# Kernel optimization log

Hardware: AMD Instinct MI355X
Metric: run time of the kernel (lower is better)

The kernel has to match this reference:

```python
import jax, jax.numpy as jnp
import numpy as np

B, S, D = 4, 2048, 512
H, DK = 8, 64
EPS = 1e-8


def setup_inputs() -> dict:
    key = jax.random.key(0)
    ks = jax.random.split(key, 11)
    sc = 1.0 / np.sqrt(D)
    Q = jax.random.normal(ks[0], (B, S, D), dtype=jnp.float32)
    # binary keep-mask over key positions, [B, S]
    attention_masks = (jax.random.uniform(ks[1], (B, S)) > 0.1).astype(jnp.float32)
    Wq = jax.random.normal(ks[2], (D, H * DK), dtype=jnp.float32) * sc
    bq = jax.random.normal(ks[3], (H * DK,), dtype=jnp.float32) * 0.01
    Wk = jax.random.normal(ks[4], (D, H * DK), dtype=jnp.float32) * sc
    bk = jax.random.normal(ks[5], (H * DK,), dtype=jnp.float32) * 0.01
    Wv = jax.random.normal(ks[6], (D, H * DK), dtype=jnp.float32) * sc
    bv = jax.random.normal(ks[7], (H * DK,), dtype=jnp.float32) * 0.01
    Wo = jax.random.normal(ks[8], (H * DK, D), dtype=jnp.float32) * (1.0 / np.sqrt(H * DK))
    bo = jax.random.normal(ks[9], (D,), dtype=jnp.float32) * 0.01
    return {"Q": Q, "attention_masks": attention_masks, "Wq": Wq, "bq": bq,
            "Wk": Wk, "bk": bk, "Wv": Wv, "bv": bv, "Wo": Wo, "bo": bo}


def reference(Q, attention_masks, Wq, bq, Wk, bk, Wv, bv, Wo, bo):
    b, s, _ = Q.shape
    # projections -> [B, H, S, DK]
    q = (Q @ Wq + bq).reshape(b, s, H, DK).transpose(0, 2, 1, 3)
    k = (Q @ Wk + bk).reshape(b, s, H, DK).transpose(0, 2, 1, 3)
    v = (Q @ Wv + bv).reshape(b, s, H, DK).transpose(0, 2, 1, 3)
    # scores: exp(QK^T / sqrt(dk)) * mask, normalized by row-sum (no max subtraction, matching source)
    scores = jnp.exp(jnp.einsum('bhqd,bhkd->bhqk', q, k) / np.sqrt(DK))
    scores = scores * attention_masks[:, None, None, :]  # mask broadcast over query dim
    attn = scores / (jnp.sum(scores, axis=-1, keepdims=True) + EPS)
    ctx = jnp.einsum('bhqk,bhkd->bhqd', attn, v)
    ctx = ctx.transpose(0, 2, 1, 3).reshape(b, s, H * DK)
    return ctx @ Wo + bo
```

## Files before the change

kernel.cpp:

```cpp
#include <hip/hip_runtime.h>
#include <math.h>

constexpr int NB = 4, NS = 2048, ND = 512, NH = 8, NDK = 64;
constexpr int NM = NB * NS, NHD = NH * NDK;

typedef short short8v __attribute__((ext_vector_type(8)));
typedef float f32x16v __attribute__((ext_vector_type(16)));
typedef unsigned int uint4v __attribute__((ext_vector_type(4)));

__device__ __forceinline__ unsigned short f2bf(float f) {
    unsigned u = __float_as_uint(f);
    return (unsigned short)((u + 0x7fffu + ((u >> 16) & 1u)) >> 16);
}
__device__ __forceinline__ float bf2f(unsigned short h) {
    return __uint_as_float(((unsigned)h) << 16);
}

#define MFMA32(a, b, c) __builtin_amdgcn_mfma_f32_32x32x16_bf16(a, b, c, 0, 0, 0)

__global__ __launch_bounds__(256) void split_x(
    const float* __restrict__ X, unsigned short* __restrict__ xh,
    unsigned short* __restrict__ xl)
{
    const size_t base = ((size_t)blockIdx.x * 256 + threadIdx.x) * 16;
#pragma unroll
    for (int j = 0; j < 4; ++j) {
        float4 v = *(const float4*)&X[base + 4 * j];
        ushort4 h, l;
        h.x = f2bf(v.x); h.y = f2bf(v.y); h.z = f2bf(v.z); h.w = f2bf(v.w);
        l.x = f2bf(v.x - bf2f(h.x)); l.y = f2bf(v.y - bf2f(h.y));
        l.z = f2bf(v.z - bf2f(h.z)); l.w = f2bf(v.w - bf2f(h.w));
        *(ushort4*)&xh[base + 4 * j] = h;
        *(ushort4*)&xl[base + 4 * j] = l;
    }
}

__global__ __launch_bounds__(256) void split_wT(
    const float* __restrict__ W0, const float* __restrict__ W1,
    const float* __restrict__ W2, const float* __restrict__ W3,
    unsigned short* __restrict__ wth, unsigned short* __restrict__ wtl)
{
    const int z = blockIdx.z;
    const float* W = (z == 0) ? W0 : (z == 1) ? W1 : (z == 2) ? W2 : W3;
    unsigned short* th = wth + (size_t)z * ND * ND;
    unsigned short* tl = wtl + (size_t)z * ND * ND;

    __shared__ float T[64][68];
    const int t = threadIdx.x;
    const int k0 = blockIdx.y * 64, n0 = blockIdx.x * 64;
    {
        const int r = t >> 2, c4 = (t & 3) * 16;
#pragma unroll
        for (int j = 0; j < 4; ++j)
            *(float4*)&T[r][c4 + 4 * j] = *(const float4*)&W[(size_t)(k0 + r) * ND + n0 + c4 + 4 * j];
    }
    __syncthreads();
    {
        const int r = t >> 2, c4 = (t & 3) * 16;
        unsigned short* dh = th + (size_t)(n0 + r) * ND + k0 + c4;
        unsigned short* dl = tl + (size_t)(n0 + r) * ND + k0 + c4;
#pragma unroll
        for (int j = 0; j < 4; ++j) {
            ushort4 h, l;
#pragma unroll
            for (int e = 0; e < 4; ++e) {
                float v = T[c4 + 4 * j + e][r];
                unsigned short hh = f2bf(v);
                ((unsigned short*)&h)[e] = hh;
                ((unsigned short*)&l)[e] = f2bf(v - bf2f(hh));
            }
            *(ushort4*)(dh + 4 * j) = h;
            *(ushort4*)(dl + 4 * j) = l;
        }
    }
}

__global__ __launch_bounds__(256, 2) void proj_qkv_mfma(
    const unsigned short* __restrict__ xh, const unsigned short* __restrict__ xl,
    const unsigned short* __restrict__ wth, const unsigned short* __restrict__ wtl,
    const float* __restrict__ bq, const float* __restrict__ bk,
    const float* __restrict__ bv,
    unsigned short* __restrict__ qh, unsigned short* __restrict__ ql,
    unsigned short* __restrict__ kh, unsigned short* __restrict__ kl,
    unsigned short* __restrict__ vh)
{
    constexpr int AH = 0, AL = 16384, BH = 32768, BL = 49152;
    __shared__ __align__(16) unsigned char smem[65536];

    const int z = blockIdx.z;
    const float* bias = (z == 0) ? bq : (z == 1) ? bk : bv;
    unsigned short* hp = (z == 0) ? qh : (z == 1) ? kh : vh;
    unsigned short* lp = (z == 0) ? ql : (z == 1) ? kl : (unsigned short*)0;
    const unsigned char* bth = (const unsigned char*)(wth + (size_t)z * ND * ND);
    const unsigned char* btl = (const unsigned char*)(wtl + (size_t)z * ND * ND);

    const int tid = threadIdx.x, lane = tid & 63, w = tid >> 6;
    const int wm = w >> 1, wn = w & 1;
    const int c = lane & 31, hi = lane >> 5;
    const int m0 = blockIdx.y * 128, n0 = blockIdx.x * 128;

    const unsigned char* ah_base = (const unsigned char*)xh;
    const unsigned char* al_base = (const unsigned char*)xl;

    int rr[4], gg[4], dd[4];
#pragma unroll
    for (int i = 0; i < 4; ++i) {
        int G = tid + 256 * i;
        rr[i] = G >> 3; gg[i] = G & 7;
        dd[i] = rr[i] * 128 + ((gg[i] ^ (rr[i] & 7)) * 16);
    }

    uint4v sah[4], sal[4], sbh[4], sbl[4];
    auto loads = [&](int kt) {
        const int kb = kt * 128;
#pragma unroll
        for (int i = 0; i < 4; ++i) {
            const size_t arow = (size_t)(m0 + rr[i]) * 1024 + kb + gg[i] * 16;
            const size_t brow = (size_t)(n0 + rr[i]) * 1024 + kb + gg[i] * 16;
            sah[i] = *(const uint4v*)(ah_base + arow);
            sal[i] = *(const uint4v*)(al_base + arow);
            sbh[i] = *(const uint4v*)(bth + brow);
            sbl[i] = *(const uint4v*)(btl + brow);
        }
    };
    auto writes = [&]() {
#pragma unroll
        for (int i = 0; i < 4; ++i) {
            *(uint4v*)(smem + AH + dd[i]) = sah[i];
            *(uint4v*)(smem + AL + dd[i]) = sal[i];
            *(uint4v*)(smem + BH + dd[i]) = sbh[i];
            *(uint4v*)(smem + BL + dd[i]) = sbl[i];
        }
    };

    f32x16v acc[2][2];
#pragma unroll
    for (int a = 0; a < 2; ++a)
#pragma unroll
        for (int bq2 = 0; bq2 < 2; ++bq2)
#pragma unroll
            for (int r = 0; r < 16; ++r) acc[a][bq2][r] = 0.f;

    loads(0);
    for (int kt = 0; kt < ND / 64; ++kt) {
        __syncthreads();
        writes();
        if (kt + 1 < ND / 64) loads(kt + 1);
        __syncthreads();
#pragma unroll
        for (int ks = 0; ks < 4; ++ks) {
            short8v afh[2], afl[2], bfh[2], bfl[2];
#pragma unroll
            for (int ms = 0; ms < 2; ++ms) {
                const int row = wm * 64 + ms * 32 + c;
                const int gb = row * 128 + (((2 * ks + hi) ^ (c & 7)) * 16);
                afh[ms] = *(const short8v*)(smem + AH + gb);
                afl[ms] = *(const short8v*)(smem + AL + gb);
            }
#pragma unroll
            for (int ns = 0; ns < 2; ++ns) {
                const int row = wn * 64 + ns * 32 + c;
                const int gb = row * 128 + (((2 * ks + hi) ^ (c & 7)) * 16);
                bfh[ns] = *(const short8v*)(smem + BH + gb);
                bfl[ns] = *(const short8v*)(smem + BL + gb);
            }
#pragma unroll
            for (int ms = 0; ms < 2; ++ms)
#pragma unroll
                for (int ns = 0; ns < 2; ++ns) {
                    acc[ms][ns] = MFMA32(afh[ms], bfh[ns], acc[ms][ns]);
                    acc[ms][ns] = MFMA32(afh[ms], bfl[ns], acc[ms][ns]);
                    acc[ms][ns] = MFMA32(afl[ms], bfh[ns], acc[ms][ns]);
                }
        }
    }

    const int b = m0 >> 11;
    const int s_base = (m0 & (NS - 1)) + wm * 64;
#pragma unroll
    for (int ns = 0; ns < 2; ++ns) {
        const int n = n0 + wn * 64 + ns * 32 + c;
        const int h = n >> 6, dk = n & (NDK - 1);
        const float bv4 = bias[n];
        const size_t bhBase = (size_t)(b * NH + h) * NS * NDK + dk;
#pragma unroll
        for (int ms = 0; ms < 2; ++ms)
#pragma unroll
            for (int r = 0; r < 16; ++r) {
                const int s = s_base + ms * 32 + (r & 3) + 8 * (r >> 2) + 4 * hi;
                const float v = acc[ms][ns][r] + bv4;
                const unsigned short h0 = f2bf(v);
                hp[bhBase + (size_t)s * NDK] = h0;
                if (lp) lp[bhBase + (size_t)s * NDK] = f2bf(v - bf2f(h0));
            }
    }
}

__global__ __launch_bounds__(256) void vt_convert(
    const unsigned short* __restrict__ vh, unsigned short* __restrict__ vth)
{
    const int bh = blockIdx.y;
    const int s0 = blockIdx.x * 64;
    __shared__ unsigned short th[64][72];
    const int t = threadIdx.x;
    {
        const int sl = t & 63, ch = (t >> 6) * 16;
        const unsigned short* sh = vh + ((size_t)bh * NS + s0 + sl) * NDK + ch;
#pragma unroll
        for (int j = 0; j < 4; ++j)
            *(ushort4*)&th[sl][ch + 4 * j] = *(const ushort4*)(sh + 4 * j);
    }
    __syncthreads();
    {
        const int dv = t >> 2, sc = (t & 3) * 16;
        unsigned short* dh = vth + ((size_t)bh * NDK + dv) * NS + s0 + sc;
#pragma unroll
        for (int j = 0; j < 4; ++j) {
            ushort4 oh;
            oh.x = th[sc + 4 * j + 0][dv]; oh.y = th[sc + 4 * j + 1][dv];
            oh.z = th[sc + 4 * j + 2][dv]; oh.w = th[sc + 4 * j + 3][dv];
            *(ushort4*)(dh + 4 * j) = oh;
        }
    }
}

__global__ __launch_bounds__(256, 2) void attn(
    const unsigned short* __restrict__ qhp, const unsigned short* __restrict__ qlp,
    const unsigned short* __restrict__ khp, const unsigned short* __restrict__ klp,
    const unsigned short* __restrict__ vthp,
    const float* __restrict__ maskp,
    unsigned short* __restrict__ cth, unsigned short* __restrict__ ctl)
{
    constexpr int KH_OFF = 0, KL_OFF = 8192, VH_OFF = 16384;
    constexpr int P_OFF = 24576;
    __shared__ __align__(16) unsigned char smem[45056];

    const int tid = threadIdx.x, lane = tid & 63, w = tid >> 6;
    const int bid = blockIdx.x;
    const int xcd = bid & 7, r0 = bid >> 3;
    const int qt = r0 & 15, bh = xcd + 8 * (r0 >> 4);
    const int b = bh >> 3;
    const int q0 = qt * 128;
    const int c = lane & 31, hi = lane >> 5;
    const int csw = (c & 7) * 16;

    unsigned* Ph = (unsigned*)(smem + P_OFF + w * 5120);
    unsigned* Pl = (unsigned*)(smem + P_OFF + w * 5120 + 2560);

    const unsigned char* kh_base = (const unsigned char*)khp + (size_t)bh * NS * 128;
    const unsigned char* kl_base = (const unsigned char*)klp + (size_t)bh * NS * 128;
    const unsigned char* vh_base = (const unsigned char*)vthp + (size_t)bh * 64 * 4096;

    const int G1 = tid, G2 = tid + 256;
    const int r1 = G1 >> 3, g1 = G1 & 7, r2 = G2 >> 3, g2 = G2 & 7;
    const int d1 = r1 * 128 + ((g1 ^ (r1 & 7)) * 16);
    const int d2 = r2 * 128 + ((g2 ^ (r2 & 7)) * 16);

    uint4v skh1, skl1, svh1, skh2, skl2, svh2;
    auto loads = [&](int kt) {
        const size_t ko = (size_t)kt * 8192;
        const size_t vo = (size_t)kt * 128;
        skh1 = *(const uint4v*)(kh_base + ko + (size_t)G1 * 16);
        skh2 = *(const uint4v*)(kh_base + ko + (size_t)G2 * 16);
        skl1 = *(const uint4v*)(kl_base + ko + (size_t)G1 * 16);
        skl2 = *(const uint4v*)(kl_base + ko + (size_t)G2 * 16);
        svh1 = *(const uint4v*)(vh_base + vo + (size_t)r1 * 4096 + g1 * 16);
        svh2 = *(const uint4v*)(vh_base + vo + (size_t)r2 * 4096 + g2 * 16);
    };
    auto writes = [&]() {
        *(uint4v*)(smem + KH_OFF + d1) = skh1;
        *(uint4v*)(smem + KH_OFF + d2) = skh2;
        *(uint4v*)(smem + KL_OFF + d1) = skl1;
        *(uint4v*)(smem + KL_OFF + d2) = skl2;
        *(uint4v*)(smem + VH_OFF + d1) = svh1;
        *(uint4v*)(smem + VH_OFF + d2) = svh2;
    };

    short8v qfh[4], qfl[4];
    {
        const unsigned short* qr  = qhp + ((size_t)bh * NS + q0 + 32 * w + c) * NDK + 8 * hi;
        const unsigned short* qrl = qlp + ((size_t)bh * NS + q0 + 32 * w + c) * NDK + 8 * hi;
#pragma unroll
        for (int km = 0; km < 4; ++km) {
            qfh[km] = *(const short8v*)(qr + km * 16);
            qfl[km] = *(const short8v*)(qrl + km * 16);
        }
    }

    f32x16v acc[2];
#pragma unroll
    for (int d = 0; d < 2; ++d)
#pragma unroll
        for (int r = 0; r < 16; ++r) acc[d][r] = 0.f;
    float dsum = 0.f;

    loads(0);
    for (int kt = 0; kt < NS / 64; ++kt) {
        __syncthreads();
        writes();
        if (kt + 1 < NS / 64) loads(kt + 1);
        __syncthreads();
#pragma unroll
        for (int kb = 0; kb < 2; ++kb) {
            short8v kfh[4], kfl[4];
            const int rowb = (32 * kb + c) * 128;
#pragma unroll
            for (int km = 0; km < 4; ++km) {
                const int gb = ((2 * km + hi) * 16) ^ csw;
                kfh[km] = *(const short8v*)(smem + KH_OFF + rowb + gb);
                kfl[km] = *(const short8v*)(smem + KL_OFF + rowb + gb);
            }
            f32x16v sacc;
#pragma unroll
            for (int r = 0; r < 16; ++r) sacc[r] = 0.f;
#pragma unroll
            for (int km = 0; km < 4; ++km) {
                sacc = MFMA32(kfh[km], qfh[km], sacc);
                sacc = MFMA32(kfh[km], qfl[km], sacc);
                sacc = MFMA32(kfl[km], qfh[km], sacc);
            }
            float pm[16];
#pragma unroll
            for (int rr2 = 0; rr2 < 4; ++rr2) {
                float4 mv = *(const float4*)&maskp[(size_t)b * NS + kt * 64 + 32 * kb + 8 * rr2 + 4 * hi];
                pm[4 * rr2 + 0] = mv.x; pm[4 * rr2 + 1] = mv.y;
                pm[4 * rr2 + 2] = mv.z; pm[4 * rr2 + 3] = mv.w;
            }
            float pf[16];
#pragma unroll
            for (int r = 0; r < 16; ++r) {
                float pv = __expf(sacc[r] * 0.125f) * pm[r];
                pf[r] = pv;
                dsum += pv;
            }
            unsigned wah[4], wbh[4], wal[4], wbl[4];
#pragma unroll
            for (int rr2 = 0; rr2 < 4; ++rr2) {
                unsigned short h0 = f2bf(pf[4 * rr2 + 0]), h1 = f2bf(pf[4 * rr2 + 1]);
                unsigned short h2 = f2bf(pf[4 * rr2 + 2]), h3 = f2bf(pf[4 * rr2 + 3]);
                wah[rr2] = (unsigned)h0 | ((unsigned)h1 << 16);
                wbh[rr2] = (unsigned)h2 | ((unsigned)h3 << 16);
                unsigned short l0 = f2bf(pf[4 * rr2 + 0] - bf2f(h0));
                unsigned short l1 = f2bf(pf[4 * rr2 + 1] - bf2f(h1));
                unsigned short l2 = f2bf(pf[4 * rr2 + 2] - bf2f(h2));
                unsigned short l3 = f2bf(pf[4 * rr2 + 3] - bf2f(h3));
                wal[rr2] = (unsigned)l0 | ((unsigned)l1 << 16);
                wbl[rr2] = (unsigned)l2 | ((unsigned)l3 << 16);
            }
#pragma unroll
            for (int rr2 = 0; rr2 < 4; ++rr2) {
                uint2 th2; th2.x = wah[rr2]; th2.y = wbh[rr2];
                uint2 tl2; tl2.x = wal[rr2]; tl2.y = wbl[rr2];
                *(uint2*)&Ph[c * 20 + 4 * rr2 + 2 * hi] = th2;
                *(uint2*)&Pl[c * 20 + 4 * rr2 + 2 * hi] = tl2;
            }
            asm volatile("s_waitcnt lgkmcnt(0)" ::: "memory");
            __builtin_amdgcn_sched_barrier(0);
#pragma unroll
            for (int pc2 = 0; pc2 < 2; ++pc2) {
                const int pc = 2 * kb + pc2;
                uint4v th4 = *(const uint4v*)&Ph[c * 20 + 8 * pc2 + 4 * hi];
                uint4v tl4 = *(const uint4v*)&Pl[c * 20 + 8 * pc2 + 4 * hi];
                short8v pfh = __builtin_bit_cast(short8v, th4);
                short8v pfl = __builtin_bit_cast(short8v, tl4);
                const int vgb = ((2 * pc + hi) * 16) ^ csw;
#pragma unroll
                for (int d = 0; d < 2; ++d) {
                    const int vrow = (32 * d + c) * 128;
                    short8v vfh = *(const short8v*)(smem + VH_OFF + vrow + vgb);
                    acc[d] = MFMA32(vfh, pfh, acc[d]);
                    acc[d] = MFMA32(vfh, pfl, acc[d]);
                }
            }
        }
    }

    dsum += __shfl_xor(dsum, 32);
    const float inv = 1.0f / (dsum + 1e-8f);
    unsigned short* ohr = cth + (size_t)bh * 64 * NS + q0 + 32 * w + c;
    unsigned short* olr = ctl + (size_t)bh * 64 * NS + q0 + 32 * w + c;
#pragma unroll
    for (int d = 0; d < 2; ++d)
#pragma unroll
        for (int r = 0; r < 16; ++r) {
            const int dv = 32 * d + (r & 3) + 8 * (r >> 2) + 4 * hi;
            const float v = acc[d][r] * inv;
            const unsigned short h0 = f2bf(v);
            ohr[(size_t)dv * NS] = h0;
            olr[(size_t)dv * NS] = f2bf(v - bf2f(h0));
        }
}

__global__ __launch_bounds__(256) void ctx_split(
    const unsigned short* __restrict__ cth, const unsigned short* __restrict__ ctl,
    unsigned short* __restrict__ cnh, unsigned short* __restrict__ cnl)
{
    const int bh = blockIdx.y;
    const int b = bh >> 3, h = bh & 7;
    const int s0 = blockIdx.x * 64;
    __shared__ unsigned short th[64][72];
    __shared__ unsigned short tl[64][72];
    const int t = threadIdx.x;
    {
        const int rd = t >> 2, sc = (t & 3) * 16;
        const unsigned short* sh = cth + ((size_t)bh * NDK + rd) * NS + s0 + sc;
        const unsigned short* sv = ctl + ((size_t)bh * NDK + rd) * NS + s0 + sc;
#pragma unroll
        for (int j = 0; j < 4; ++j) {
            *(ushort4*)&th[rd][sc + 4 * j] = *(const ushort4*)(sh + 4 * j);
            *(ushort4*)&tl[rd][sc + 4 * j] = *(const ushort4*)(sv + 4 * j);
        }
    }
    __syncthreads();
    {
        const int sl = t >> 2, kc = (t & 3) * 16;
        const size_t m = (size_t)b * NS + s0 + sl;
        unsigned short* dh = cnh + m * NHD + h * NDK + kc;
        unsigned short* dl = cnl + m * NHD + h * NDK + kc;
#pragma unroll
        for (int j = 0; j < 4; ++j) {
            ushort4 hh, ll;
#pragma unroll
            for (int e = 0; e < 4; ++e) {
                hh_e_assign:;
                ((unsigned short*)&hh)[e] = th[kc + 4 * j + e][sl];
                ((unsigned short*)&ll)[e] = tl[kc + 4 * j + e][sl];
            }
            *(ushort4*)(dh + 4 * j) = hh;
            *(ushort4*)(dl + 4 * j) = ll;
        }
    }
}

__global__ __launch_bounds__(256, 2) void proj_out_mfma(
    const unsigned short* __restrict__ cnh, const unsigned short* __restrict__ cnl,
    const unsigned short* __restrict__ wth, const unsigned short* __restrict__ wtl,
    const float* __restrict__ bo, float* __restrict__ out)
{
    constexpr int AH = 0, AL = 16384, BH = 32768, BL = 49152;
    __shared__ __align__(16) unsigned char smem[65536];

    const int tid = threadIdx.x, lane = tid & 63, w = tid >> 6;
    const int wm = w >> 1, wn = w & 1;
    const int c = lane & 31, hi = lane >> 5;
    const int m0 = blockIdx.y * 128, n0 = blockIdx.x * 128;

    const unsigned char* ah_base = (const unsigned char*)cnh;
    const unsigned char* al_base = (const unsigned char*)cnl;
    const unsigned char* bth = (const unsigned char*)wth;
    const unsigned char* btl = (const unsigned char*)wtl;

    int rr[4], gg[4], dd[4];
#pragma unroll
    for (int i = 0; i < 4; ++i) {
        int G = tid + 256 * i;
        rr[i] = G >> 3; gg[i] = G & 7;
        dd[i] = rr[i] * 128 + ((gg[i] ^ (rr[i] & 7)) * 16);
    }

    uint4v sah[4], sal[4], sbh[4], sbl[4];
    auto loads = [&](int kt) {
        const int kb = kt * 128;
#pragma unroll
        for (int i = 0; i < 4; ++i) {
            const size_t arow = (size_t)(m0 + rr[i]) * 1024 + kb + gg[i] * 16;
            const size_t brow = (size_t)(n0 + rr[i]) * 1024 + kb + gg[i] * 16;
            sah[i] = *(const uint4v*)(ah_base + arow);
            sal[i] = *(const uint4v*)(al_base + arow);
            sbh[i] = *(const uint4v*)(bth + brow);
            sbl[i] = *(const uint4v*)(btl + brow);
        }
    };
    auto writes = [&]() {
#pragma unroll
        for (int i = 0; i < 4; ++i) {
            *(uint4v*)(smem + AH + dd[i]) = sah[i];
            *(uint4v*)(smem + AL + dd[i]) = sal[i];
            *(uint4v*)(smem + BH + dd[i]) = sbh[i];
            *(uint4v*)(smem + BL + dd[i]) = sbl[i];
        }
    };

    f32x16v acc[2][2];
#pragma unroll
    for (int a = 0; a < 2; ++a)
#pragma unroll
        for (int bq2 = 0; bq2 < 2; ++bq2)
#pragma unroll
            for (int r = 0; r < 16; ++r) acc[a][bq2][r] = 0.f;

    loads(0);
    for (int kt = 0; kt < NHD / 64; ++kt) {
        __syncthreads();
        writes();
        if (kt + 1 < NHD / 64) loads(kt + 1);
        __syncthreads();
#pragma unroll
        for (int ks = 0; ks < 4; ++ks) {
            short8v afh[2], afl[2], bfh[2], bfl[2];
#pragma unroll
            for (int ms = 0; ms < 2; ++ms) {
                const int row = wm * 64 + ms * 32 + c;
                const int gb = row * 128 + (((2 * ks + hi) ^ (c & 7)) * 16);
                afh[ms] = *(const short8v*)(smem + AH + gb);
                afl[ms] = *(const short8v*)(smem + AL + gb);
            }
#pragma unroll
            for (int ns = 0; ns < 2; ++ns) {
                const int row = wn * 64 + ns * 32 + c;
                const int gb = row * 128 + (((2 * ks + hi) ^ (c & 7)) * 16);
                bfh[ns] = *(const short8v*)(smem + BH + gb);
                bfl[ns] = *(const short8v*)(smem + BL + gb);
            }
#pragma unroll
            for (int ms = 0; ms < 2; ++ms)
#pragma unroll
                for (int ns = 0; ns < 2; ++ns) {
                    acc[ms][ns] = MFMA32(afh[ms], bfh[ns], acc[ms][ns]);
                    acc[ms][ns] = MFMA32(afh[ms], bfl[ns], acc[ms][ns]);
                    acc[ms][ns] = MFMA32(afl[ms], bfh[ns], acc[ms][ns]);
                }
        }
    }

#pragma unroll
    for (int ns = 0; ns < 2; ++ns) {
        const int n = n0 + wn * 64 + ns * 32 + c;
        const float bv4 = bo[n];
#pragma unroll
        for (int ms = 0; ms < 2; ++ms)
#pragma unroll
            for (int r = 0; r < 16; ++r) {
                const int m = m0 + wm * 64 + ms * 32 + (r & 3) + 8 * (r >> 2) + 4 * hi;
                out[(size_t)m * ND + n] = acc[ms][ns][r] + bv4;
            }
    }
}

extern "C" void kernel_launch(void* const* d_in, const int* in_sizes, int n_in,
                              void* d_out, int out_size, void* d_ws, size_t ws_size,
                              hipStream_t stream) {
    const float* Q    = (const float*)d_in[0];
    const float* mask = (const float*)d_in[1];
    const float* Wq   = (const float*)d_in[2];
    const float* bq   = (const float*)d_in[3];
    const float* Wk   = (const float*)d_in[4];
    const float* bk   = (const float*)d_in[5];
    const float* Wv   = (const float*)d_in[6];
    const float* bv   = (const float*)d_in[7];
    const float* Wo   = (const float*)d_in[8];
    const float* bo   = (const float*)d_in[9];

    unsigned char* W = (unsigned char*)d_ws;
    constexpr size_t MB = 1048576;
    unsigned short* xh   = (unsigned short*)(W + 0);
    unsigned short* xl   = (unsigned short*)(W + 8 * MB);
    unsigned short* wtH  = (unsigned short*)(W + 16 * MB);
    unsigned short* wtL  = (unsigned short*)(W + 18 * MB);
    unsigned short* qh   = (unsigned short*)(W + 20 * MB);
    unsigned short* ql   = (unsigned short*)(W + 28 * MB);
    unsigned short* kh   = (unsigned short*)(W + 36 * MB);
    unsigned short* kl   = (unsigned short*)(W + 44 * MB);
    unsigned short* vh   = (unsigned short*)(W + 52 * MB);
    unsigned short* vth  = (unsigned short*)(W + 0);
    unsigned short* cth  = (unsigned short*)(W + 8 * MB);
    unsigned short* ctl  = (unsigned short*)(W + 52 * MB);
    unsigned short* cnh  = (unsigned short*)(W + 20 * MB);
    unsigned short* cnl  = (unsigned short*)(W + 28 * MB);

    split_x<<<NM * ND / (256 * 16), 256, 0, stream>>>(Q, xh, xl);
    split_wT<<<dim3(8, 8, 4), 256, 0, stream>>>(Wq, Wk, Wv, Wo, wtH, wtL);

    proj_qkv_mfma<<<dim3(NHD / 128, NM / 128, 3), 256, 0, stream>>>(
        xh, xl, wtH, wtL, bq, bk, bv, qh, ql, kh, kl, vh);

    vt_convert<<<dim3(NS / 64, NB * NH), 256, 0, stream>>>(vh, vth);

    attn<<<512, 256, 0, stream>>>(qh, ql, kh, kl, vth, mask, cth, ctl);

    ctx_split<<<dim3(NS / 64, NB * NH), 256, 0, stream>>>(cth, ctl, cnh, cnl);

    proj_out_mfma<<<dim3(ND / 128, NM / 128), 256, 0, stream>>>(
        cnh, cnl, wtH + (size_t)3 * ND * ND, wtL + (size_t)3 * ND * ND,
        bo, (float*)d_out);
}
```

Baseline: 279.4 us.

## Drop low-half bf16 split for P and context, double-buffer attention K/V tiles

The attention kernel now stores probabilities only as a single bf16 value and runs one PV MFMA per tile instead of two. The context output drops its low part, so ctx_split and the output projection move only the high half and run two MFMAs per step instead of three. The K/V shared-memory staging is double-buffered, leaving one barrier per tile instead of two, and exp is computed via exp2f with a prescaled constant. The aim is to cut MFMA count, LDS traffic and memory bandwidth, at the cost of lower numerical accuracy and more shared memory per block.

```diff
diff --git a/kernel.cpp b/kernel.cpp
--- a/kernel.cpp
+++ b/kernel.cpp
@@ -229,11 +229,12 @@
     const unsigned short* __restrict__ khp, const unsigned short* __restrict__ klp,
     const unsigned short* __restrict__ vthp,
     const float* __restrict__ maskp,
-    unsigned short* __restrict__ cth, unsigned short* __restrict__ ctl)
-{
-    constexpr int KH_OFF = 0, KL_OFF = 8192, VH_OFF = 16384;
-    constexpr int P_OFF = 24576;
-    __shared__ __align__(16) unsigned char smem[45056];
+    unsigned short* __restrict__ cth)
+{
+    constexpr int NT = NS / 64;
+    constexpr int KH = 0, KL = 8192, VH = 16384, TILE = 24576;
+    constexpr int P_OFF = 49152;
+    __shared__ __align__(16) unsigned char smem[59392];
 
     const int tid = threadIdx.x, lane = tid & 63, w = tid >> 6;
     const int bid = blockIdx.x;
@@ -244,8 +245,7 @@
     const int c = lane & 31, hi = lane >> 5;
     const int csw = (c & 7) * 16;
 
-    unsigned* Ph = (unsigned*)(smem + P_OFF + w * 5120);
-    unsigned* Pl = (unsigned*)(smem + P_OFF + w * 5120 + 2560);
+    unsigned* Ph = (unsigned*)(smem + P_OFF + w * 2560);
 
     const unsigned char* kh_base = (const unsigned char*)khp + (size_t)bh * NS * 128;
     const unsigned char* kl_base = (const unsigned char*)klp + (size_t)bh * NS * 128;
@@ -267,13 +267,13 @@
         svh1 = *(const uint4v*)(vh_base + vo + (size_t)r1 * 4096 + g1 * 16);
         svh2 = *(const uint4v*)(vh_base + vo + (size_t)r2 * 4096 + g2 * 16);
     };
-    auto writes = [&]() {
-        *(uint4v*)(smem + KH_OFF + d1) = skh1;
-        *(uint4v*)(smem + KH_OFF + d2) = skh2;
-        *(uint4v*)(smem + KL_OFF + d1) = skl1;
-        *(uint4v*)(smem + KL_OFF + d2) = skl2;
-        *(uint4v*)(smem + VH_OFF + d1) = svh1;
-        *(uint4v*)(smem + VH_OFF + d2) = svh2;
+    auto writes = [&](unsigned char* buf) {
+        *(uint4v*)(buf + KH + d1) = skh1;
+        *(uint4v*)(buf + KH + d2) = skh2;
+        *(uint4v*)(buf + KL + d1) = skl1;
+        *(uint4v*)(buf + KL + d2) = skl2;
+        *(uint4v*)(buf + VH + d1) = svh1;
+        *(uint4v*)(buf + VH + d2) = svh2;
     };
 
     short8v qfh[4], qfl[4];
@@ -294,12 +294,7 @@
         for (int r = 0; r < 16; ++r) acc[d][r] = 0.f;
     float dsum = 0.f;
 
-    loads(0);
-    for (int kt = 0; kt < NS / 64; ++kt) {
-        __syncthreads();
-        writes();
-        if (kt + 1 < NS / 64) loads(kt + 1);
-        __syncthreads();
+    auto compute = [&](const unsigned char* buf, int kt) {
 #pragma unroll
         for (int kb = 0; kb < 2; ++kb) {
             short8v kfh[4], kfl[4];
@@ -307,8 +302,8 @@
 #pragma unroll
             for (int km = 0; km < 4; ++km) {
                 const int gb = ((2 * km + hi) * 16) ^ csw;
-                kfh[km] = *(const short8v*)(smem + KH_OFF + rowb + gb);
-                kfl[km] = *(const short8v*)(smem + KL_OFF + rowb + gb);
+                kfh[km] = *(const short8v*)(buf + KH + rowb + gb);
+                kfl[km] = *(const short8v*)(buf + KL + rowb + gb);
             }
             f32x16v sacc;
 #pragma unroll
@@ -326,33 +321,23 @@
                 pm[4 * rr2 + 0] = mv.x; pm[4 * rr2 + 1] = mv.y;
                 pm[4 * rr2 + 2] = mv.z; pm[4 * rr2 + 3] = mv.w;
             }
-            float pf[16];
+            unsigned short hh[16];
 #pragma unroll
             for (int r = 0; r < 16; ++r) {
-                float pv = __expf(sacc[r] * 0.125f) * pm[r];
-                pf[r] = pv;
-                dsum += pv;
-            }
-            unsigned wah[4], wbh[4], wal[4], wbl[4];
+                float pv = exp2f(sacc[r] * 0.18033688011112042f) * pm[r];
+                hh[r] = f2bf(pv);
+                dsum += bf2f(hh[r]);
+            }
+            unsigned wah[4], wbh[4];
 #pragma unroll
             for (int rr2 = 0; rr2 < 4; ++rr2) {
-                unsigned short h0 = f2bf(pf[4 * rr2 + 0]), h1 = f2bf(pf[4 * rr2 + 1]);
-                unsigned short h2 = f2bf(pf[4 * rr2 + 2]), h3 = f2bf(pf[4 * rr2 + 3]);
-                wah[rr2] = (unsigned)h0 | ((unsigned)h1 << 16);
-                wbh[rr2] = (unsigned)h2 | ((unsigned)h3 << 16);
-                unsigned short l0 = f2bf(pf[4 * rr2 + 0] - bf2f(h0));
-                unsigned short l1 = f2bf(pf[4 * rr2 + 1] - bf2f(h1));
-                unsigned short l2 = f2bf(pf[4 * rr2 + 2] - bf2f(h2));
-                unsigned short l3 = f2bf(pf[4 * rr2 + 3] - bf2f(h3));
-                wal[rr2] = (unsigned)l0 | ((unsigned)l1 << 16);
-                wbl[rr2] = (unsigned)l2 | ((unsigned)l3 << 16);
+                wah[rr2] = (unsigned)hh[4 * rr2 + 0] | ((unsigned)hh[4 * rr2 + 1] << 16);
+                wbh[rr2] = (unsigned)hh[4 * rr2 + 2] | ((unsigned)hh[4 * rr2 + 3] << 16);
             }
 #pragma unroll
             for (int rr2 = 0; rr2 < 4; ++rr2) {
                 uint2 th2; th2.x = wah[rr2]; th2.y = wbh[rr2];
-                uint2 tl2; tl2.x = wal[rr2]; tl2.y = wbl[rr2];
                 *(uint2*)&Ph[c * 20 + 4 * rr2 + 2 * hi] = th2;
-                *(uint2*)&Pl[c * 20 + 4 * rr2 + 2 * hi] = tl2;
             }
             asm volatile("s_waitcnt lgkmcnt(0)" ::: "memory");
             __builtin_amdgcn_sched_barrier(0);
@@ -360,85 +345,87 @@
             for (int pc2 = 0; pc2 < 2; ++pc2) {
                 const int pc = 2 * kb + pc2;
                 uint4v th4 = *(const uint4v*)&Ph[c * 20 + 8 * pc2 + 4 * hi];
-                uint4v tl4 = *(const uint4v*)&Pl[c * 20 + 8 * pc2 + 4 * hi];
                 short8v pfh = __builtin_bit_cast(short8v, th4);
-                short8v pfl = __builtin_bit_cast(short8v, tl4);
                 const int vgb = ((2 * pc + hi) * 16) ^ csw;
 #pragma unroll
                 for (int d = 0; d < 2; ++d) {
                     const int vrow = (32 * d + c) * 128;
-                    short8v vfh = *(const short8v*)(smem + VH_OFF + vrow + vgb);
+                    short8v vfh = *(const short8v*)(buf + VH + vrow + vgb);
                     acc[d] = MFMA32(vfh, pfh, acc[d]);
-                    acc[d] = MFMA32(vfh, pfl, acc[d]);
                 }
             }
         }
+    };
+
+    unsigned char* buf0 = smem;
+    unsigned char* buf1 = smem + TILE;
+
+    loads(0);
+    writes(buf0);
+    loads(1);
+    __syncthreads();
+
+    auto step = [&](int kt, unsigned char* rbuf, unsigned char* wbuf) {
+        if (kt + 1 < NT) writes(wbuf);
+        if (kt + 2 < NT) loads(kt + 2);
+        compute(rbuf, kt);
+        __syncthreads();
+    };
+    for (int kt = 0; kt < NT; kt += 2) {
+        step(kt, buf0, buf1);
+        step(kt + 1, buf1, buf0);
     }
 
     dsum += __shfl_xor(dsum, 32);
     const float inv = 1.0f / (dsum + 1e-8f);
     unsigned short* ohr = cth + (size_t)bh * 64 * NS + q0 + 32 * w + c;
-    unsigned short* olr = ctl + (size_t)bh * 64 * NS + q0 + 32 * w + c;
 #pragma unroll
     for (int d = 0; d < 2; ++d)
 #pragma unroll
         for (int r = 0; r < 16; ++r) {
             const int dv = 32 * d + (r & 3) + 8 * (r >> 2) + 4 * hi;
-            const float v = acc[d][r] * inv;
-            const unsigned short h0 = f2bf(v);
-            ohr[(size_t)dv * NS] = h0;
-            olr[(size_t)dv * NS] = f2bf(v - bf2f(h0));
+            ohr[(size_t)dv * NS] = f2bf(acc[d][r] * inv);
         }
 }
 
 __global__ __launch_bounds__(256) void ctx_split(
-    const unsigned short* __restrict__ cth, const unsigned short* __restrict__ ctl,
-    unsigned short* __restrict__ cnh, unsigned short* __restrict__ cnl)
+    const unsigned short* __restrict__ cth, unsigned short* __restrict__ cnh)
 {
     const int bh = blockIdx.y;
     const int b = bh >> 3, h = bh & 7;
     const int s0 = blockIdx.x * 64;
     __shared__ unsigned short th[64][72];
-    __shared__ unsigned short tl[64][72];
     const int t = threadIdx.x;
     {
         const int rd = t >> 2, sc = (t & 3) * 16;
         const unsigned short* sh = cth + ((size_t)bh * NDK + rd) * NS + s0 + sc;
-        const unsigned short* sv = ctl + ((size_t)bh * NDK + rd) * NS + s0 + sc;
-#pragma unroll
-        for (int j = 0; j < 4; ++j) {
+#pragma unroll
+        for (int j = 0; j < 4; ++j)
             *(ushort4*)&th[rd][sc + 4 * j] = *(const ushort4*)(sh + 4 * j);
-            *(ushort4*)&tl[rd][sc + 4 * j] = *(const ushort4*)(sv + 4 * j);
-        }
     }
     __syncthreads();
     {
         const int sl = t >> 2, kc = (t & 3) * 16;
         const size_t m = (size_t)b * NS + s0 + sl;
         unsigned short* dh = cnh + m * NHD + h * NDK + kc;
-        unsigned short* dl = cnl + m * NHD + h * NDK + kc;
 #pragma unroll
         for (int j = 0; j < 4; ++j) {
-            ushort4 hh, ll;
-#pragma unroll
-            for (int e = 0; e < 4; ++e) {
-                hh_e_assign:;
+            ushort4 hh;
+#pragma unroll
+            for (int e = 0; e < 4; ++e)
                 ((unsigned short*)&hh)[e] = th[kc + 4 * j + e][sl];
-                ((unsigned short*)&ll)[e] = tl[kc + 4 * j + e][sl];
-            }
             *(ushort4*)(dh + 4 * j) = hh;
-            *(ushort4*)(dl + 4 * j) = ll;
         }
     }
 }
 
 __global__ __launch_bounds__(256, 2) void proj_out_mfma(
-    const unsigned short* __restrict__ cnh, const unsigned short* __restrict__ cnl,
+    const unsigned short* __restrict__ cnh,
     const unsigned short* __restrict__ wth, const unsigned short* __restrict__ wtl,
     const float* __restrict__ bo, float* __restrict__ out)
 {
-    constexpr int AH = 0, AL = 16384, BH = 32768, BL = 49152;
-    __shared__ __align__(16) unsigned char smem[65536];
+    constexpr int AH = 0, BH = 16384, BL = 32768;
+    __shared__ __align__(16) unsigned char smem[49152];
 
     const int tid = threadIdx.x, lane = tid & 63, w = tid >> 6;
     const int wm = w >> 1, wn = w & 1;
@@ -446,7 +433,6 @@
     const int m0 = blockIdx.y * 128, n0 = blockIdx.x * 128;
 
     const unsigned char* ah_base = (const unsigned char*)cnh;
-    const unsigned char* al_base = (const unsigned char*)cnl;
     const unsigned char* bth = (const unsigned char*)wth;
     const unsigned char* btl = (const unsigned char*)wtl;
 
@@ -458,7 +444,7 @@
         dd[i] = rr[i] * 128 + ((gg[i] ^ (rr[i] & 7)) * 16);
     }
 
-    uint4v sah[4], sal[4], sbh[4], sbl[4];
+    uint4v sah[4], sbh[4], sbl[4];
     auto loads = [&](int kt) {
         const int kb = kt * 128;
 #pragma unroll
@@ -466,7 +452,6 @@
             const size_t arow = (size_t)(m0 + rr[i]) * 1024 + kb + gg[i] * 16;
             const size_t brow = (size_t)(n0 + rr[i]) * 1024 + kb + gg[i] * 16;
             sah[i] = *(const uint4v*)(ah_base + arow);
-            sal[i] = *(const uint4v*)(al_base + arow);
             sbh[i] = *(const uint4v*)(bth + brow);
             sbl[i] = *(const uint4v*)(btl + brow);
         }
@@ -475,7 +460,6 @@
 #pragma unroll
         for (int i = 0; i < 4; ++i) {
             *(uint4v*)(smem + AH + dd[i]) = sah[i];
-            *(uint4v*)(smem + AL + dd[i]) = sal[i];
             *(uint4v*)(smem + BH + dd[i]) = sbh[i];
             *(uint4v*)(smem + BL + dd[i]) = sbl[i];
         }
@@ -497,13 +481,12 @@
         __syncthreads();
 #pragma unroll
         for (int ks = 0; ks < 4; ++ks) {
-            short8v afh[2], afl[2], bfh[2], bfl[2];
+            short8v afh[2], bfh[2], bfl[2];
 #pragma unroll
             for (int ms = 0; ms < 2; ++ms) {
                 const int row = wm * 64 + ms * 32 + c;
                 const int gb = row * 128 + (((2 * ks + hi) ^ (c & 7)) * 16);
                 afh[ms] = *(const short8v*)(smem + AH + gb);
-                afl[ms] = *(const short8v*)(smem + AL + gb);
             }
 #pragma unroll
             for (int ns = 0; ns < 2; ++ns) {
@@ -518,7 +501,6 @@
                 for (int ns = 0; ns < 2; ++ns) {
                     acc[ms][ns] = MFMA32(afh[ms], bfh[ns], acc[ms][ns]);
                     acc[ms][ns] = MFMA32(afh[ms], bfl[ns], acc[ms][ns]);
-                    acc[ms][ns] = MFMA32(afl[ms], bfh[ns], acc[ms][ns]);
                 }
         }
     }
@@ -564,9 +546,7 @@
     unsigned short* vh   = (unsigned short*)(W + 52 * MB);
     unsigned short* vth  = (unsigned short*)(W + 0);
     unsigned short* cth  = (unsigned short*)(W + 8 * MB);
-    unsigned short* ctl  = (unsigned short*)(W + 52 * MB);
     unsigned short* cnh  = (unsigned short*)(W + 20 * MB);
-    unsigned short* cnl  = (unsigned short*)(W + 28 * MB);
 
     split_x<<<NM * ND / (256 * 16), 256, 0, stream>>>(Q, xh, xl);
     split_wT<<<dim3(8, 8, 4), 256, 0, stream>>>(Wq, Wk, Wv, Wo, wtH, wtL);
@@ -576,11 +556,11 @@
 
     vt_convert<<<dim3(NS / 64, NB * NH), 256, 0, stream>>>(vh, vth);
 
-    attn<<<512, 256, 0, stream>>>(qh, ql, kh, kl, vth, mask, cth, ctl);
-
-    ctx_split<<<dim3(NS / 64, NB * NH), 256, 0, stream>>>(cth, ctl, cnh, cnl);
+    attn<<<512, 256, 0, stream>>>(qh, ql, kh, kl, vth, mask, cth);
+
+    ctx_split<<<dim3(NS / 64, NB * NH), 256, 0, stream>>>(cth, cnh);
 
     proj_out_mfma<<<dim3(ND / 128, NM / 128), 256, 0, stream>>>(
-        cnh, cnl, wtH + (size_t)3 * ND * ND, wtL + (size_t)3 * ND * ND,
+        cnh, wtH + (size_t)3 * ND * ND, wtL + (size_t)3 * ND * ND,
         bo, (float*)d_out);
 }
```

After: 262.9 us. 1.06x faster.
